# Optimization experiments

Hardware: AMD Instinct MI355X
Metric: run time of the kernel (lower is better)

The kernel has to match this reference:

```python
import jax, jax.numpy as jnp
import numpy as np

N = 100000   # nodes
DEG = 16     # neighbors per node (uniform CSR)
E = N * DEG  # edges
D = 64       # node feature dim
COORD = 2    # coord_dim used for attention
EPS = 1e-9


def setup_inputs() -> dict:
    key = jax.random.key(0)
    k1, k2, k3, k4 = jax.random.split(key, 4)
    y = jax.random.normal(k1, (N, D), dtype=jnp.float32)
    indices = jax.random.randint(k2, (E,), 0, N, dtype=jnp.int64)
    indptr = (jnp.arange(N + 1, dtype=jnp.int64) * DEG)
    W1 = jax.random.normal(k3, (2 * D, 128), dtype=jnp.float32) * (1.0 / np.sqrt(2 * D))
    b1 = jnp.zeros((128,), dtype=jnp.float32)
    W2 = jax.random.normal(k4, (128, 64), dtype=jnp.float32) * (1.0 / np.sqrt(128))
    b2 = jnp.zeros((64,), dtype=jnp.float32)
    return {"y": y, "indices": indices, "indptr": indptr,
            "W1": W1, "b1": b1, "W2": W2, "b2": b2}


def _csr_repeat_ids(indptr, num_edges):
    # segids[e] = i such that indptr[i] <= e < indptr[i+1]
    return jnp.searchsorted(indptr, jnp.arange(num_edges, dtype=indptr.dtype), side='right') - 1


def _segment_softmax(s, segids, nsegs):
    smax = jax.ops.segment_max(s, segids, num_segments=nsegs)
    e = jnp.exp(s - smax[segids])
    denom = jax.ops.segment_sum(e, segids, num_segments=nsegs)
    return e / denom[segids]


def reference(y, indices, indptr, W1, b1, W2, b2):
    nsegs = y.shape[0]
    num_edges = indices.shape[0]
    segids = _csr_repeat_ids(indptr, num_edges)       # [E]

    rep_y = y[indices]                                # neighbor gather  [E, D]
    self_x = y[segids]                                # == repeat(x, num_reps) since x is y  [E, D]

    # cosine attention on coordinate slice
    qx = self_x[:, :COORD]
    ky = rep_y[:, :COORD]
    qn = qx / jnp.clip(jnp.linalg.norm(qx, axis=-1, keepdims=True), EPS)
    kn = ky / jnp.clip(jnp.linalg.norm(ky, axis=-1, keepdims=True), EPS)
    s = jnp.sum(qn * kn, axis=-1)                     # [E]
    a = _segment_softmax(s, segids, nsegs)            # [E]

    agg = jnp.concatenate([rep_y, self_x], axis=-1)   # [E, 2D]
    h = jax.nn.relu(agg @ W1 + b1)                    # [E, 128]
    m = h @ W2 + b2                                   # [E, 64]

    m = m * a[:, None]
    out = jax.ops.segment_sum(m, segids, num_segments=nsegs)  # [N, 64]
    return out
```

## Files before the change

kernel.cpp:

```cpp
#include <hip/hip_runtime.h>
#include <cstdint>

#define DEG 16
#define NNODE 100000
#define NTILE 3125
#define NT64 1563

typedef _Float16 f16;
typedef _Float16 h2v  __attribute__((ext_vector_type(2)));
typedef _Float16 f16x8 __attribute__((ext_vector_type(8)));
typedef float    f32x4 __attribute__((ext_vector_type(4)));

union U4 { uint4 u; h2v h[4]; f16x8 v; };
union U1 { uint32_t i; h2v h; };

__device__ __forceinline__ h2v pk2h(float a, float b) {
    auto r = __builtin_amdgcn_cvt_pkrtz(a, b);
    h2v o;
    __builtin_memcpy(&o, &r, sizeof(o));
    return o;
}

__device__ __host__ __forceinline__ int kperm(int p) {
    return (p & 0xC3) | ((p & 0x0C) << 2) | ((p & 0x30) >> 2);
}

__global__ __launch_bounds__(256) void k_prep(
    const float* __restrict__ W1, const float* __restrict__ W2,
    f16* __restrict__ W1A, f16* __restrict__ W2A)
{
    const int g0 = blockIdx.x * 256 + threadIdx.x;
    for (int i = g0; i < 16384 + 8192; i += 24 * 256) {
        if (i < 16384) {
            const int j = i & 7, lane = (i >> 3) & 63, kb = (i >> 9) & 1, mt = i >> 10;
            const int m = 16 * mt + (lane & 15);
            const int k = kb * 32 + (lane >> 4) * 8 + j;
            const int row = (m < 128) ? k : (64 + k);
            const int col = m & 127;
            W1A[i] = (f16)W1[row * 128 + col];
        } else {
            const int ii = i - 16384;
            const int j = ii & 7, lane = (ii >> 3) & 63, kb = (ii >> 9) & 3, mt = ii >> 11;
            const int c = 16 * mt + (lane & 15);
            const int p = kb * 32 + (lane >> 4) * 8 + j;
            W2A[ii] = (f16)W2[kperm(p) * 64 + c];
        }
    }
}

__global__ __launch_bounds__(256, 4) void k_uv(
    const float* __restrict__ y, const f16* __restrict__ W1A,
    const float* __restrict__ b1,
    unsigned char* __restrict__ U8, f16* __restrict__ Vh, float2* __restrict__ QN)
{
    __shared__ float ysh[4096];
    const int t = threadIdx.x;
    const long nbase = (long)blockIdx.x * 64;
    const int lane = t & 63;
    const int w = t >> 6;
    const int c16 = lane & 15, q = lane >> 4;

    {
        const size_t max4 = (size_t)NNODE * 16;
        char* yb = (char*)ysh;
        #pragma unroll
        for (int i = 0; i < 4; ++i) {
            const int e = t + i * 256;
            size_t gidx = (size_t)blockIdx.x * 1024 + e;
            if (gidx >= max4) gidx = max4 - 1;
            const float4 v = ((const float4*)y)[gidx];
            const int B = e * 16;
            const int row = B >> 8;
            *(float4*)(yb + (B ^ ((row & 7) << 4))) = v;
        }
    }

    if (QN != nullptr && t < 64) {
        const long node = nbase + t;
        if (node < NNODE) {
            const float qx = y[node * 64], qy = y[node * 64 + 1];
            const float n = fmaxf(sqrtf(qx * qx + qy * qy), 1e-9f);
            QN[node] = make_float2(qx / n, qy / n);
        }
    }
    __syncthreads();

    const char* yb = (const char*)ysh;
    f16x8 bf[4][2];
    #pragma unroll
    for (int nt = 0; nt < 4; ++nt) {
        const int r = 16 * nt + c16;
        const int sw = (r & 7) << 4;
        #pragma unroll
        for (int kb = 0; kb < 2; ++kb) {
            const int base = r * 256 + kb * 128 + q * 32;
            const float4 a = *(const float4*)(yb + (base ^ sw));
            const float4 b = *(const float4*)(yb + ((base + 16) ^ sw));
            U4 rg;
            rg.h[0] = pk2h(a.x, a.y);
            rg.h[1] = pk2h(a.z, a.w);
            rg.h[2] = pk2h(b.x, b.y);
            rg.h[3] = pk2h(b.z, b.w);
            bf[nt][kb] = rg.v;
        }
    }

    f32x4 acc[4][4];
    #pragma unroll
    for (int i = 0; i < 4; ++i)
        #pragma unroll
        for (int nt = 0; nt < 4; ++nt)
            acc[i][nt] = (f32x4){0.f, 0.f, 0.f, 0.f};

    #pragma unroll
    for (int i = 0; i < 4; ++i) {
        const int mt = 4 * w + i;
        #pragma unroll
        for (int kb = 0; kb < 2; ++kb) {
            const f16x8 af = *(const f16x8*)&W1A[((mt * 2 + kb) * 64 + lane) * 8];
            #pragma unroll
            for (int nt = 0; nt < 4; ++nt)
                acc[i][nt] = __builtin_amdgcn_mfma_f32_16x16x32_f16(af, bf[nt][kb], acc[i][nt], 0, 0, 0);
        }
    }

    const bool isV = (w >= 2);
    const int wef = w & 1;
    float4 b1v[4];
    #pragma unroll
    for (int i = 0; i < 4; ++i) b1v[i] = make_float4(0.f, 0.f, 0.f, 0.f);
    if (isV) {
        #pragma unroll
        for (int i = 0; i < 4; ++i)
            b1v[i] = *(const float4*)&b1[wef * 64 + 16 * i + 4 * q];
    }

    #pragma unroll
    for (int nt = 0; nt < 4; ++nt) {
        const long node = nbase + 16 * nt + c16;
        if (node >= NNODE) continue;
        if (!isV) {
            uint4 pkt;
            uint32_t wd[4];
            #pragma unroll
            for (int i = 0; i < 4; ++i) {
                uint32_t v0 = __builtin_amdgcn_cvt_pk_fp8_f32(acc[i][nt][0], acc[i][nt][1], 0, false);
                wd[i] = __builtin_amdgcn_cvt_pk_fp8_f32(acc[i][nt][2], acc[i][nt][3], v0, true);
            }
            pkt.x = wd[0]; pkt.y = wd[1]; pkt.z = wd[2]; pkt.w = wd[3];
            *(uint4*)(U8 + node * 128 + wef * 64 + q * 16) = pkt;
        } else {
            f16* dst = Vh + node * 128 + wef * 64 + q * 16;
            U4 p0, p1;
            p0.h[0] = pk2h(acc[0][nt][0] + b1v[0].x, acc[0][nt][1] + b1v[0].y);
            p0.h[1] = pk2h(acc[0][nt][2] + b1v[0].z, acc[0][nt][3] + b1v[0].w);
            p0.h[2] = pk2h(acc[1][nt][0] + b1v[1].x, acc[1][nt][1] + b1v[1].y);
            p0.h[3] = pk2h(acc[1][nt][2] + b1v[1].z, acc[1][nt][3] + b1v[1].w);
            p1.h[0] = pk2h(acc[2][nt][0] + b1v[2].x, acc[2][nt][1] + b1v[2].y);
            p1.h[1] = pk2h(acc[2][nt][2] + b1v[2].z, acc[2][nt][3] + b1v[2].w);
            p1.h[2] = pk2h(acc[3][nt][0] + b1v[3].x, acc[3][nt][1] + b1v[3].y);
            p1.h[3] = pk2h(acc[3][nt][2] + b1v[3].z, acc[3][nt][3] + b1v[3].w);
            *(uint4*)dst       = p0.u;
            *(uint4*)(dst + 8) = p1.u;
        }
    }
}

template<bool USE_QN>
__global__ __launch_bounds__(256, 6) void k_agg(
    const float* __restrict__ y, const int* __restrict__ idx,
    const unsigned char* __restrict__ U8, const f16* __restrict__ Vh,
    const float2* __restrict__ QN, const f16* __restrict__ W2A,
    const float* __restrict__ b2, float* __restrict__ out)
{
    __shared__ uint32_t accs[2048];

    const int t = threadIdx.x, lane = t & 63, wave = t >> 6;
    const int c16 = lane & 15, quarter = lane >> 4;
    const int nodeBase = blockIdx.x * 32 + wave * 8;

    int jA[8];
    #pragma unroll
    for (int g = 0; g < 8; ++g)
        jA[g] = idx[(nodeBase + g) * DEG + c16];

    float aA[8];
    #pragma unroll
    for (int g = 0; g < 8; ++g) {
        const int i = nodeBase + g;
        float s;
        if (USE_QN) {
            const float2 qn = QN[i];
            const float2 kn = QN[jA[g]];
            s = qn.x * kn.x + qn.y * kn.y;
        } else {
            const float2 qv = *(const float2*)&y[(long)i * 64];
            const float2 kv = *(const float2*)&y[(long)jA[g] * 64];
            const float nq = fmaxf(sqrtf(qv.x * qv.x + qv.y * qv.y), 1e-9f);
            const float nk = fmaxf(sqrtf(kv.x * kv.x + kv.y * kv.y), 1e-9f);
            s = (qv.x * kv.x + qv.y * kv.y) / (nq * nk);
        }
        float m = s;
        #pragma unroll
        for (int d = 1; d < 16; d <<= 1) m = fmaxf(m, __shfl_xor(m, d));
        const float ex = __expf(s - m);
        float sum = ex;
        #pragma unroll
        for (int d = 1; d < 16; d <<= 1) sum += __shfl_xor(sum, d);
        aA[g] = ex / sum;
    }

    const uint2* Uv = (const uint2*)U8;
    const uint4* Vv = (const uint4*)Vh;
    char* accb = (char*)accs;

    uint2 ub[2][4];
    U4 vb[2];
    vb[0].u = Vv[(long)nodeBase * 16 + c16];
    #pragma unroll
    for (int ee = 0; ee < 4; ++ee) {
        const long je = __shfl(jA[0], 4 * ee + quarter);
        ub[0][ee] = Uv[je * 16 + c16];
    }

    #pragma unroll
    for (int g = 0; g < 8; ++g) {
        const int cur = g & 1, nx = cur ^ 1;
        if (g < 7) {
            vb[nx].u = Vv[(long)(nodeBase + g + 1) * 16 + c16];
            #pragma unroll
            for (int ee = 0; ee < 4; ++ee) {
                const long je = __shfl(jA[g + 1], 4 * ee + quarter);
                ub[nx][ee] = Uv[je * 16 + c16];
            }
        }
        const h2v z2 = {0, 0};
        h2v r0 = {0, 0}, r1 = {0, 0}, r2 = {0, 0}, r3 = {0, 0};
        #pragma unroll
        for (int ee = 0; ee < 4; ++ee) {
            const float ae = __shfl(aA[g], 4 * ee + quarter);
            const h2v az = pk2h(ae, ae);
            const uint2 uu = ub[cur][ee];
            auto q01 = __builtin_amdgcn_cvt_pk_f32_fp8(uu.x, false);
            auto q23 = __builtin_amdgcn_cvt_pk_f32_fp8(uu.x, true);
            auto q45 = __builtin_amdgcn_cvt_pk_f32_fp8(uu.y, false);
            auto q67 = __builtin_amdgcn_cvt_pk_f32_fp8(uu.y, true);
            const h2v u0 = pk2h(q01[0], q01[1]);
            const h2v u1 = pk2h(q23[0], q23[1]);
            const h2v u2 = pk2h(q45[0], q45[1]);
            const h2v u3 = pk2h(q67[0], q67[1]);
            r0 += __builtin_elementwise_max(u0 + vb[cur].h[0], z2) * az;
            r1 += __builtin_elementwise_max(u1 + vb[cur].h[1], z2) * az;
            r2 += __builtin_elementwise_max(u2 + vb[cur].h[2], z2) * az;
            r3 += __builtin_elementwise_max(u3 + vb[cur].h[3], z2) * az;
        }
        h2v rr[4] = {r0, r1, r2, r3};
        #pragma unroll
        for (int p = 0; p < 4; ++p) {
            U1 v; v.h = rr[p];
            U1 o; o.i = __shfl_xor(v.i, 16); v.h = v.h + o.h;
            o.i = __shfl_xor(v.i, 32);       v.h = v.h + o.h;
            rr[p] = v.h;
        }
        if (quarter == 0) {
            const int rrow = wave * 8 + g;
            U4 pk; pk.h[0] = rr[0]; pk.h[1] = rr[1]; pk.h[2] = rr[2]; pk.h[3] = rr[3];
            *(uint4*)(accb + ((rrow * 256 + c16 * 16) ^ ((rrow & 7) << 4))) = pk.u;
        }
    }
    __syncthreads();

    f16x8 waf[4];
    #pragma unroll
    for (int kb = 0; kb < 4; ++kb)
        waf[kb] = *(const f16x8*)&W2A[((wave * 4 + kb) * 64 + lane) * 8];
    const float4 b2v = *(const float4*)&b2[16 * wave + quarter * 4];

    f32x4 d[2];
    #pragma unroll
    for (int nt = 0; nt < 2; ++nt) d[nt] = (f32x4){0.f, 0.f, 0.f, 0.f};
    #pragma unroll
    for (int nt = 0; nt < 2; ++nt) {
        const int n = 16 * nt + c16;
        const int sw = (n & 7) << 4;
        #pragma unroll
        for (int kb = 0; kb < 4; ++kb) {
            const f16x8 bfr = *(const f16x8*)(accb + ((n * 256 + kb * 64 + quarter * 16) ^ sw));
            d[nt] = __builtin_amdgcn_mfma_f32_16x16x32_f16(waf[kb], bfr, d[nt], 0, 0, 0);
        }
    }
    #pragma unroll
    for (int nt = 0; nt < 2; ++nt) {
        const long node = blockIdx.x * 32 + 16 * nt + c16;
        const int col = 16 * wave + quarter * 4;
        float4 o;
        o.x = d[nt][0] + b2v.x; o.y = d[nt][1] + b2v.y;
        o.z = d[nt][2] + b2v.z; o.w = d[nt][3] + b2v.w;
        *(float4*)&out[node * 64 + col] = o;
    }
}

extern "C" void kernel_launch(void* const* d_in, const int* in_sizes, int n_in,
                              void* d_out, int out_size, void* d_ws, size_t ws_size,
                              hipStream_t stream) {
    const float* y   = (const float*)d_in[0];
    const int*   idx = (const int*)d_in[1];
    const float* W1  = (const float*)d_in[3];
    const float* b1  = (const float*)d_in[4];
    const float* W2  = (const float*)d_in[5];
    const float* b2  = (const float*)d_in[6];
    float* out = (float*)d_out;

    char* ws = (char*)d_ws;
    unsigned char* U8 = (unsigned char*)ws;
    f16* Vh  = (f16*)(ws + 12800000);
    f16* W1A = (f16*)(ws + 38400000);
    f16* W2A = (f16*)(ws + 38432768);
    const size_t qn_off = 38449152;
    const bool useQN = (ws_size >= qn_off + (size_t)NNODE * sizeof(float2));
    float2* QN = useQN ? (float2*)(ws + qn_off) : nullptr;

    k_prep<<<24, 256, 0, stream>>>(W1, W2, W1A, W2A);
    k_uv<<<NT64, 256, 0, stream>>>(y, W1A, b1, U8, Vh, QN);
    if (useQN)
        k_agg<true><<<NTILE, 256, 0, stream>>>(y, idx, U8, Vh, QN, W2A, b2, out);
    else
        k_agg<false><<<NTILE, 256, 0, stream>>>(y, idx, U8, Vh, nullptr, W2A, b2, out);
}
```

Baseline: 65.47 us.

## Compute self-projection V inside aggregation kernel instead of storing to global

Moves the self-node half of the first MLP layer (y·W1_bottom + b1) out of k_uv and into k_agg. Each aggregation block now computes V for its 32 nodes with MFMA and keeps it in shared memory, so the 25.6 MB fp16 Vh buffer is never written or read back. k_uv now only produces the fp8 neighbor projections, with its work redistributed across the four waves. In exchange, k_agg needs more shared memory and registers (occupancy hint lowered from 6 to 4), adds an extra __syncthreads, and re-reads y.

```diff
diff --git a/kernel.cpp b/kernel.cpp
--- a/kernel.cpp
+++ b/kernel.cpp
@@ -12,6 +12,7 @@
 typedef float    f32x4 __attribute__((ext_vector_type(4)));
 
 union U4 { uint4 u; h2v h[4]; f16x8 v; };
+union U2u { uint2 u; h2v h[2]; };
 union U1 { uint32_t i; h2v h; };
 
 __device__ __forceinline__ h2v pk2h(float a, float b) {
@@ -50,8 +51,7 @@
 
 __global__ __launch_bounds__(256, 4) void k_uv(
     const float* __restrict__ y, const f16* __restrict__ W1A,
-    const float* __restrict__ b1,
-    unsigned char* __restrict__ U8, f16* __restrict__ Vh, float2* __restrict__ QN)
+    unsigned char* __restrict__ U8, float2* __restrict__ QN)
 {
     __shared__ float ysh[4096];
     const int t = threadIdx.x;
@@ -105,16 +105,17 @@
         }
     }
 
-    f32x4 acc[4][4];
-    #pragma unroll
-    for (int i = 0; i < 4; ++i)
+    const int mtbase = 4 * (w & 1) + 2 * (w >> 1);
+    f32x4 acc[2][4];
+    #pragma unroll
+    for (int i = 0; i < 2; ++i)
         #pragma unroll
         for (int nt = 0; nt < 4; ++nt)
             acc[i][nt] = (f32x4){0.f, 0.f, 0.f, 0.f};
 
     #pragma unroll
-    for (int i = 0; i < 4; ++i) {
-        const int mt = 4 * w + i;
+    for (int i = 0; i < 2; ++i) {
+        const int mt = mtbase + i;
         #pragma unroll
         for (int kb = 0; kb < 2; ++kb) {
             const f16x8 af = *(const f16x8*)&W1A[((mt * 2 + kb) * 64 + lane) * 8];
@@ -124,56 +125,34 @@
         }
     }
 
-    const bool isV = (w >= 2);
-    const int wef = w & 1;
-    float4 b1v[4];
-    #pragma unroll
-    for (int i = 0; i < 4; ++i) b1v[i] = make_float4(0.f, 0.f, 0.f, 0.f);
-    if (isV) {
-        #pragma unroll
-        for (int i = 0; i < 4; ++i)
-            b1v[i] = *(const float4*)&b1[wef * 64 + 16 * i + 4 * q];
-    }
-
+    const int pbase = 64 * (w & 1) + 16 * q + 8 * (w >> 1);
     #pragma unroll
     for (int nt = 0; nt < 4; ++nt) {
         const long node = nbase + 16 * nt + c16;
         if (node >= NNODE) continue;
-        if (!isV) {
-            uint4 pkt;
-            uint32_t wd[4];
-            #pragma unroll
-            for (int i = 0; i < 4; ++i) {
-                uint32_t v0 = __builtin_amdgcn_cvt_pk_fp8_f32(acc[i][nt][0], acc[i][nt][1], 0, false);
-                wd[i] = __builtin_amdgcn_cvt_pk_fp8_f32(acc[i][nt][2], acc[i][nt][3], v0, true);
-            }
-            pkt.x = wd[0]; pkt.y = wd[1]; pkt.z = wd[2]; pkt.w = wd[3];
-            *(uint4*)(U8 + node * 128 + wef * 64 + q * 16) = pkt;
-        } else {
-            f16* dst = Vh + node * 128 + wef * 64 + q * 16;
-            U4 p0, p1;
-            p0.h[0] = pk2h(acc[0][nt][0] + b1v[0].x, acc[0][nt][1] + b1v[0].y);
-            p0.h[1] = pk2h(acc[0][nt][2] + b1v[0].z, acc[0][nt][3] + b1v[0].w);
-            p0.h[2] = pk2h(acc[1][nt][0] + b1v[1].x, acc[1][nt][1] + b1v[1].y);
-            p0.h[3] = pk2h(acc[1][nt][2] + b1v[1].z, acc[1][nt][3] + b1v[1].w);
-            p1.h[0] = pk2h(acc[2][nt][0] + b1v[2].x, acc[2][nt][1] + b1v[2].y);
-            p1.h[1] = pk2h(acc[2][nt][2] + b1v[2].z, acc[2][nt][3] + b1v[2].w);
-            p1.h[2] = pk2h(acc[3][nt][0] + b1v[3].x, acc[3][nt][1] + b1v[3].y);
-            p1.h[3] = pk2h(acc[3][nt][2] + b1v[3].z, acc[3][nt][3] + b1v[3].w);
-            *(uint4*)dst       = p0.u;
-            *(uint4*)(dst + 8) = p1.u;
-        }
+        uint32_t d0, d1;
+        {
+            uint32_t v0 = __builtin_amdgcn_cvt_pk_fp8_f32(acc[0][nt][0], acc[0][nt][1], 0, false);
+            d0 = __builtin_amdgcn_cvt_pk_fp8_f32(acc[0][nt][2], acc[0][nt][3], v0, true);
+            uint32_t v1 = __builtin_amdgcn_cvt_pk_fp8_f32(acc[1][nt][0], acc[1][nt][1], 0, false);
+            d1 = __builtin_amdgcn_cvt_pk_fp8_f32(acc[1][nt][2], acc[1][nt][3], v1, true);
+        }
+        uint2 pk; pk.x = d0; pk.y = d1;
+        *(uint2*)(U8 + node * 128 + pbase) = pk;
     }
 }
 
 template<bool USE_QN>
-__global__ __launch_bounds__(256, 6) void k_agg(
+__global__ __launch_bounds__(256, 4) void k_agg(
     const float* __restrict__ y, const int* __restrict__ idx,
-    const unsigned char* __restrict__ U8, const f16* __restrict__ Vh,
-    const float2* __restrict__ QN, const f16* __restrict__ W2A,
-    const float* __restrict__ b2, float* __restrict__ out)
+    const unsigned char* __restrict__ U8,
+    const float2* __restrict__ QN,
+    const f16* __restrict__ W1A, const f16* __restrict__ W2A,
+    const float* __restrict__ b1, const float* __restrict__ b2,
+    float* __restrict__ out)
 {
     __shared__ uint32_t accs[2048];
+    __shared__ uint32_t vshs[2048];
 
     const int t = threadIdx.x, lane = t & 63, wave = t >> 6;
     const int c16 = lane & 15, quarter = lane >> 4;
@@ -183,6 +162,50 @@
     #pragma unroll
     for (int g = 0; g < 8; ++g)
         jA[g] = idx[(nodeBase + g) * DEG + c16];
+
+    const int h = wave & 1;
+    const int vnt = wave >> 1;
+    const long vnode = (long)blockIdx.x * 32 + 16 * vnt + c16;
+
+    f16x8 bfv[2];
+    #pragma unroll
+    for (int kb = 0; kb < 2; ++kb) {
+        const float4 a = *(const float4*)&y[vnode * 64 + kb * 32 + quarter * 8];
+        const float4 b = *(const float4*)&y[vnode * 64 + kb * 32 + quarter * 8 + 4];
+        U4 rg;
+        rg.h[0] = pk2h(a.x, a.y);
+        rg.h[1] = pk2h(a.z, a.w);
+        rg.h[2] = pk2h(b.x, b.y);
+        rg.h[3] = pk2h(b.z, b.w);
+        bfv[kb] = rg.v;
+    }
+
+    f32x4 vacc[4];
+    #pragma unroll
+    for (int i = 0; i < 4; ++i) vacc[i] = (f32x4){0.f, 0.f, 0.f, 0.f};
+    #pragma unroll
+    for (int i = 0; i < 4; ++i) {
+        const int mt = 8 + 4 * h + i;
+        #pragma unroll
+        for (int kb = 0; kb < 2; ++kb) {
+            const f16x8 af = *(const f16x8*)&W1A[((mt * 2 + kb) * 64 + lane) * 8];
+            vacc[i] = __builtin_amdgcn_mfma_f32_16x16x32_f16(af, bfv[kb], vacc[i], 0, 0, 0);
+        }
+    }
+
+    char* vsb = (char*)vshs;
+    {
+        const int vrow = 16 * vnt + c16;
+        const int vsw = (vrow & 7) << 4;
+        #pragma unroll
+        for (int i = 0; i < 4; ++i) {
+            const float4 bv = *(const float4*)&b1[64 * h + 16 * i + 4 * quarter];
+            U2u pk;
+            pk.h[0] = pk2h(vacc[i][0] + bv.x, vacc[i][1] + bv.y);
+            pk.h[1] = pk2h(vacc[i][2] + bv.z, vacc[i][3] + bv.w);
+            *(uint2*)(vsb + ((vrow * 256 + h * 128 + quarter * 32 + i * 8) ^ vsw)) = pk.u;
+        }
+    }
 
     float aA[8];
     #pragma unroll
@@ -210,13 +233,12 @@
         aA[g] = ex / sum;
     }
 
+    __syncthreads();
+
     const uint2* Uv = (const uint2*)U8;
-    const uint4* Vv = (const uint4*)Vh;
     char* accb = (char*)accs;
 
     uint2 ub[2][4];
-    U4 vb[2];
-    vb[0].u = Vv[(long)nodeBase * 16 + c16];
     #pragma unroll
     for (int ee = 0; ee < 4; ++ee) {
         const long je = __shfl(jA[0], 4 * ee + quarter);
@@ -227,13 +249,16 @@
     for (int g = 0; g < 8; ++g) {
         const int cur = g & 1, nx = cur ^ 1;
         if (g < 7) {
-            vb[nx].u = Vv[(long)(nodeBase + g + 1) * 16 + c16];
             #pragma unroll
             for (int ee = 0; ee < 4; ++ee) {
                 const long je = __shfl(jA[g + 1], 4 * ee + quarter);
                 ub[nx][ee] = Uv[je * 16 + c16];
             }
         }
+        const int vrow = wave * 8 + g;
+        U4 vfr;
+        vfr.u = *(const uint4*)(vsb + ((vrow * 256 + c16 * 16) ^ ((vrow & 7) << 4)));
+
         const h2v z2 = {0, 0};
         h2v r0 = {0, 0}, r1 = {0, 0}, r2 = {0, 0}, r3 = {0, 0};
         #pragma unroll
@@ -249,10 +274,10 @@
             const h2v u1 = pk2h(q23[0], q23[1]);
             const h2v u2 = pk2h(q45[0], q45[1]);
             const h2v u3 = pk2h(q67[0], q67[1]);
-            r0 += __builtin_elementwise_max(u0 + vb[cur].h[0], z2) * az;
-            r1 += __builtin_elementwise_max(u1 + vb[cur].h[1], z2) * az;
-            r2 += __builtin_elementwise_max(u2 + vb[cur].h[2], z2) * az;
-            r3 += __builtin_elementwise_max(u3 + vb[cur].h[3], z2) * az;
+            r0 += __builtin_elementwise_max(u0 + vfr.h[0], z2) * az;
+            r1 += __builtin_elementwise_max(u1 + vfr.h[1], z2) * az;
+            r2 += __builtin_elementwise_max(u2 + vfr.h[2], z2) * az;
+            r3 += __builtin_elementwise_max(u3 + vfr.h[3], z2) * az;
         }
         h2v rr[4] = {r0, r1, r2, r3};
         #pragma unroll
@@ -313,17 +338,16 @@
 
     char* ws = (char*)d_ws;
     unsigned char* U8 = (unsigned char*)ws;
-    f16* Vh  = (f16*)(ws + 12800000);
-    f16* W1A = (f16*)(ws + 38400000);
-    f16* W2A = (f16*)(ws + 38432768);
-    const size_t qn_off = 38449152;
+    f16* W1A = (f16*)(ws + 12800000);
+    f16* W2A = (f16*)(ws + 12832768);
+    const size_t qn_off = 12849152;
     const bool useQN = (ws_size >= qn_off + (size_t)NNODE * sizeof(float2));
     float2* QN = useQN ? (float2*)(ws + qn_off) : nullptr;
 
     k_prep<<<24, 256, 0, stream>>>(W1, W2, W1A, W2A);
-    k_uv<<<NT64, 256, 0, stream>>>(y, W1A, b1, U8, Vh, QN);
+    k_uv<<<NT64, 256, 0, stream>>>(y, W1A, U8, QN);
     if (useQN)
-        k_agg<true><<<NTILE, 256, 0, stream>>>(y, idx, U8, Vh, QN, W2A, b2, out);
+        k_agg<true><<<NTILE, 256, 0, stream>>>(y, idx, U8, QN, W1A, W2A, b1, b2, out);
     else
-        k_agg<false><<<NTILE, 256, 0, stream>>>(y, idx, U8, Vh, nullptr, W2A, b2, out);
-}
+        k_agg<false><<<NTILE, 256, 0, stream>>>(y, idx, U8, nullptr, W1A, W2A, b1, b2, out);
+}
```

Measured after the change: 66.06 us. No clear change (+0.9%).
